# Kernel tuning notes

Measured on AMD Instinct MI355X. Metric: run time of the kernel, lower is better.

The kernel has to match this reference:

```python
import jax, jax.numpy as jnp
import numpy as np


def setup_inputs() -> dict:
    key = jax.random.key(0)
    k1, k2 = jax.random.split(key)
    B, L, D = 16, 512, 256
    text_features = jax.random.normal(k1, (B, L, D), dtype=jnp.float32)
    durations = jax.random.randint(k2, (B, L), 0, 32, dtype=jnp.int64)
    return {"text_features": text_features, "durations": durations, "target_length": 8192}


def reference(text_features, durations, target_length):
    """Length-regulator: expand [B,L,d] phoneme features to [B,T,d] frames.

    Frame t of batch b copies phoneme p where cumsum(dur)[b,p-1] <= t < cumsum(dur)[b,p];
    frames past the total duration are zero (matches torch zeros-init + trim/pad to
    target_length, since padding with the last frame only occurs when the buffer was
    already target_length long in the original code path with target_length set).
    """
    B, L, D = text_features.shape
    T = target_length  # static python int -> jit-friendly fixed output length
    cum = jnp.cumsum(durations, axis=1)                      # [B, L]
    t = jnp.arange(T, dtype=cum.dtype)                       # [T]
    # first phoneme index p with cum[b,p] > t  (side='right')
    idx = jax.vmap(lambda c: jnp.searchsorted(c, t, side='right'))(cum)  # [B, T]
    idx = jnp.minimum(idx, L - 1)
    valid = t[None, :] < cum[:, -1:]                         # [B, T] frames within total dur
    gathered = jnp.take_along_axis(text_features, idx[:, :, None], axis=1)  # [B, T, D]
    return jnp.where(valid[:, :, None], gathered, jnp.zeros((), dtype=text_features.dtype))
```

## Files before the change

kernel.cpp:

```cpp
#include <hip/hip_runtime.h>

#define MAX_L 2048
#define MAX_EPC 8
#define FRAMES_PER_BLOCK 64

__global__ __launch_bounds__(256, 3) void lr_fused_kernel(
        const float* __restrict__ feat,
        const int* __restrict__ dur,
        const int* __restrict__ tlen,
        float* __restrict__ out,
        int BL, int BT, int D) {
    const int T = *tlen;
    const int B = BT / T;
    const int L = BL / B;
    const int vecs = D >> 2;

    __shared__ int sc[MAX_L];
    __shared__ int swsum[4];
    __shared__ int sidx[FRAMES_PER_BLOCK];

    const int frame_base = blockIdx.x * FRAMES_PER_BLOCK;
    if (frame_base >= BT) return;
    const int b  = frame_base / T;
    const int t0 = frame_base - b * T;

    const int tid  = threadIdx.x;
    const int lane = tid & 63;
    const int wv   = tid >> 6;

    const int epc  = (L + blockDim.x - 1) / blockDim.x;
    const int base = tid * epc;
    const int* __restrict__ drow = dur + (size_t)b * L;

    int local[MAX_EPC];
    int run = 0;
#pragma unroll
    for (int e = 0; e < MAX_EPC; ++e) {
        int v = 0;
        if (e < epc && base + e < L) v = drow[base + e];
        run += v;
        local[e] = run;
    }
    int ws = run;
#pragma unroll
    for (int off = 1; off < 64; off <<= 1) {
        int up = __shfl_up(ws, off, 64);
        if (lane >= off) ws += up;
    }
    if (lane == 63) swsum[wv] = ws;
    __syncthreads();
    int wprefix = 0;
    for (int w = 0; w < wv; ++w) wprefix += swsum[w];
    const int chunk_prefix = wprefix + ws - run;
#pragma unroll
    for (int e = 0; e < MAX_EPC; ++e) {
        if (e < epc && base + e < L) sc[base + e] = chunk_prefix + local[e];
    }
    __syncthreads();

    const int total = sc[L - 1];

    if (tid < FRAMES_PER_BLOCK) {
        const int t = t0 + tid;
        int p = -1;
        if (t < total && frame_base + tid < BT) {
            int lo = 0, hi = L - 1;
            while (lo < hi) {
                const int mid = (lo + hi) >> 1;
                if (sc[mid] > t) hi = mid;
                else             lo = mid + 1;
            }
            p = lo;
        }
        sidx[tid] = p;
    }
    __syncthreads();

    const float4 z = make_float4(0.f, 0.f, 0.f, 0.f);

    if (vecs == 64) {
        const float4* __restrict__ fb = (const float4*)(feat + (size_t)b * L * D);
        float4* __restrict__ ob = (float4*)(out + (size_t)frame_base * D);
#pragma unroll
        for (int j = 0; j < 16; ++j) {
            const int f  = wv * 16 + j;
            const int pj = sidx[f];
            float4 v = z;
            if (pj >= 0) v = fb[(size_t)pj * 64 + lane];
            ob[(size_t)f * 64 + lane] = v;
        }
    } else {
        const float4* __restrict__ fb = (const float4*)(feat + (size_t)b * L * D);
        float4* __restrict__ ob = (float4*)(out + (size_t)frame_base * D);
        for (int j = 0; j < 16; ++j) {
            const int f = wv * 16 + j;
            if (frame_base + f >= BT) continue;
            const int pj = sidx[f];
            float4* __restrict__ orow = ob + (size_t)f * vecs;
            if (pj >= 0) {
                const float4* __restrict__ irow = fb + (size_t)pj * vecs;
                for (int i = lane; i < vecs; i += 64) orow[i] = irow[i];
            } else {
                for (int i = lane; i < vecs; i += 64) orow[i] = z;
            }
        }
    }
}

extern "C" void kernel_launch(void* const* d_in, const int* in_sizes, int n_in,
                              void* d_out, int out_size, void* d_ws, size_t ws_size,
                              hipStream_t stream) {
    const float* feat = (const float*)d_in[0];
    const int*   dur  = (const int*)d_in[1];
    const int*   tlen = (const int*)d_in[2];

    const int BL = in_sizes[1];
    const int D  = in_sizes[0] / in_sizes[1];
    const int BT = out_size / D;

    const int grid = (BT + FRAMES_PER_BLOCK - 1) / FRAMES_PER_BLOCK;
    lr_fused_kernel<<<grid, 256, 0, stream>>>(feat, dur, tlen, (float*)d_out,
                                              BL, BT, D);
}
```

Measured before the change: 147.8 us.

## Split into index kernel and grid-stride float4 gather copy kernel

Splits the fused kernel in two. The first kernel computes the per-frame source row index: one frame per thread, with 256 frames per block so the prefix scan is shared across more frames. The second kernel does a flat grid-stride gather copy with 4-way unrolled float4 loads over a fixed grid of 2048 blocks. This cuts redundant per-block cumsum work and raises memory-level parallelism in the copy, at the cost of an extra launch and writing and reading the index array through global memory.

```diff
diff --git a/kernel.cpp b/kernel.cpp
--- a/kernel.cpp
+++ b/kernel.cpp
@@ -2,24 +2,20 @@
 
 #define MAX_L 2048
 #define MAX_EPC 8
-#define FRAMES_PER_BLOCK 64
 
-__global__ __launch_bounds__(256, 3) void lr_fused_kernel(
-        const float* __restrict__ feat,
+__global__ __launch_bounds__(256) void lr_index_kernel(
         const int* __restrict__ dur,
         const int* __restrict__ tlen,
-        float* __restrict__ out,
-        int BL, int BT, int D) {
+        int* __restrict__ widx,
+        int BL, int BT) {
     const int T = *tlen;
     const int B = BT / T;
     const int L = BL / B;
-    const int vecs = D >> 2;
 
     __shared__ int sc[MAX_L];
     __shared__ int swsum[4];
-    __shared__ int sidx[FRAMES_PER_BLOCK];
 
-    const int frame_base = blockIdx.x * FRAMES_PER_BLOCK;
+    const int frame_base = blockIdx.x * 256;
     if (frame_base >= BT) return;
     const int b  = frame_base / T;
     const int t0 = frame_base - b * T;
@@ -53,57 +49,74 @@
     for (int w = 0; w < wv; ++w) wprefix += swsum[w];
     const int chunk_prefix = wprefix + ws - run;
 #pragma unroll
-    for (int e = 0; e < MAX_EPC; ++e) {
+    for (int e = 0; e < MAX_EPC; ++e)
         if (e < epc && base + e < L) sc[base + e] = chunk_prefix + local[e];
-    }
     __syncthreads();
 
     const int total = sc[L - 1];
 
-    if (tid < FRAMES_PER_BLOCK) {
+    const int f = frame_base + tid;
+    if (f < BT) {
         const int t = t0 + tid;
         int p = -1;
-        if (t < total && frame_base + tid < BT) {
+        if (t < total) {
             int lo = 0, hi = L - 1;
             while (lo < hi) {
                 const int mid = (lo + hi) >> 1;
                 if (sc[mid] > t) hi = mid;
                 else             lo = mid + 1;
             }
-            p = lo;
+            p = b * L + lo;
         }
-        sidx[tid] = p;
+        widx[f] = p;
     }
-    __syncthreads();
+}
 
+__global__ __launch_bounds__(256) void lr_copy_kernel(
+        const float4* __restrict__ fb,
+        const int* __restrict__ widx,
+        float4* __restrict__ ob,
+        long n, int shift) {
+    const long stride = (long)gridDim.x * blockDim.x;
+    const int  mask   = (1 << shift) - 1;
     const float4 z = make_float4(0.f, 0.f, 0.f, 0.f);
 
-    if (vecs == 64) {
-        const float4* __restrict__ fb = (const float4*)(feat + (size_t)b * L * D);
-        float4* __restrict__ ob = (float4*)(out + (size_t)frame_base * D);
-#pragma unroll
-        for (int j = 0; j < 16; ++j) {
-            const int f  = wv * 16 + j;
-            const int pj = sidx[f];
-            float4 v = z;
-            if (pj >= 0) v = fb[(size_t)pj * 64 + lane];
-            ob[(size_t)f * 64 + lane] = v;
-        }
-    } else {
-        const float4* __restrict__ fb = (const float4*)(feat + (size_t)b * L * D);
-        float4* __restrict__ ob = (float4*)(out + (size_t)frame_base * D);
-        for (int j = 0; j < 16; ++j) {
-            const int f = wv * 16 + j;
-            if (frame_base + f >= BT) continue;
-            const int pj = sidx[f];
-            float4* __restrict__ orow = ob + (size_t)f * vecs;
-            if (pj >= 0) {
-                const float4* __restrict__ irow = fb + (size_t)pj * vecs;
-                for (int i = lane; i < vecs; i += 64) orow[i] = irow[i];
-            } else {
-                for (int i = lane; i < vecs; i += 64) orow[i] = z;
-            }
-        }
+    long g = (long)blockIdx.x * blockDim.x + threadIdx.x;
+    for (; g + 3 * stride < n; g += 4 * stride) {
+        const long g0 = g, g1 = g + stride, g2 = g + 2 * stride, g3 = g + 3 * stride;
+        const int r0 = widx[g0 >> shift];
+        const int r1 = widx[g1 >> shift];
+        const int r2 = widx[g2 >> shift];
+        const int r3 = widx[g3 >> shift];
+        float4 v0 = fb[((long)max(r0, 0) << shift) + (int)(g0 & mask)];
+        float4 v1 = fb[((long)max(r1, 0) << shift) + (int)(g1 & mask)];
+        float4 v2 = fb[((long)max(r2, 0) << shift) + (int)(g2 & mask)];
+        float4 v3 = fb[((long)max(r3, 0) << shift) + (int)(g3 & mask)];
+        ob[g0] = (r0 >= 0) ? v0 : z;
+        ob[g1] = (r1 >= 0) ? v1 : z;
+        ob[g2] = (r2 >= 0) ? v2 : z;
+        ob[g3] = (r3 >= 0) ? v3 : z;
+    }
+    for (; g < n; g += stride) {
+        const int r = widx[g >> shift];
+        float4 v = fb[((long)max(r, 0) << shift) + (int)(g & mask)];
+        ob[g] = (r >= 0) ? v : z;
+    }
+}
+
+__global__ __launch_bounds__(256) void lr_copy_generic_kernel(
+        const float4* __restrict__ fb,
+        const int* __restrict__ widx,
+        float4* __restrict__ ob,
+        long n, int vecs) {
+    const long stride = (long)gridDim.x * blockDim.x;
+    const float4 z = make_float4(0.f, 0.f, 0.f, 0.f);
+    for (long g = (long)blockIdx.x * blockDim.x + threadIdx.x; g < n; g += stride) {
+        const long frame = g / vecs;
+        const int  off   = (int)(g - frame * vecs);
+        const int  r     = widx[frame];
+        float4 v = fb[(long)max(r, 0) * vecs + off];
+        ob[g] = (r >= 0) ? v : z;
     }
 }
 
@@ -117,8 +130,25 @@
     const int BL = in_sizes[1];
     const int D  = in_sizes[0] / in_sizes[1];
     const int BT = out_size / D;
+    const int vecs = D >> 2;
 
-    const int grid = (BT + FRAMES_PER_BLOCK - 1) / FRAMES_PER_BLOCK;
-    lr_fused_kernel<<<grid, 256, 0, stream>>>(feat, dur, tlen, (float*)d_out,
-                                              BL, BT, D);
+    int* widx = (int*)d_ws;
+
+    const int grid1 = (BT + 255) / 256;
+    lr_index_kernel<<<grid1, 256, 0, stream>>>(dur, tlen, widx, BL, BT);
+
+    const long n = (long)BT * vecs;
+    int shift = -1;
+    if ((vecs & (vecs - 1)) == 0) {
+        shift = 0;
+        while ((1 << shift) != vecs) ++shift;
+    }
+    const int grid2 = 2048;
+    if (shift >= 0) {
+        lr_copy_kernel<<<grid2, 256, 0, stream>>>(
+            (const float4*)feat, widx, (float4*)d_out, n, shift);
+    } else {
+        lr_copy_generic_kernel<<<grid2, 256, 0, stream>>>(
+            (const float4*)feat, widx, (float4*)d_out, n, vecs);
+    }
 }
```

Result: slower. 185.3 us (+25.3%).

## Double frames per block and reuse loaded rows across repeated phoneme indices

Applied to the files above, without the earlier changes.

Each block now handles 128 frames instead of 64, which halves the number of blocks that each recompute the per-batch duration prefix scan. The fast path broadcasts each frame's phoneme index with readlane and reloads the feature row only when the index changes, cutting redundant global reads for consecutive frames that map to the same phoneme. Blocks can now span a batch boundary through a segment loop. The occupancy hint in launch_bounds was removed, and with fewer blocks the GPU has less parallelism to hide memory latency.

```diff
diff --git a/kernel.cpp b/kernel.cpp
--- a/kernel.cpp
+++ b/kernel.cpp
@@ -2,9 +2,9 @@
 
 #define MAX_L 2048
 #define MAX_EPC 8
-#define FRAMES_PER_BLOCK 64
+#define FPB 128
 
-__global__ __launch_bounds__(256, 3) void lr_fused_kernel(
+__global__ __launch_bounds__(256) void lr_fused_kernel(
         const float* __restrict__ feat,
         const int* __restrict__ dur,
         const int* __restrict__ tlen,
@@ -17,93 +17,107 @@
 
     __shared__ int sc[MAX_L];
     __shared__ int swsum[4];
-    __shared__ int sidx[FRAMES_PER_BLOCK];
+    __shared__ int sidx[FPB];
 
-    const int frame_base = blockIdx.x * FRAMES_PER_BLOCK;
-    if (frame_base >= BT) return;
-    const int b  = frame_base / T;
-    const int t0 = frame_base - b * T;
+    const long frame_base0 = (long)blockIdx.x * FPB;
+    if (frame_base0 >= BT) return;
 
     const int tid  = threadIdx.x;
     const int lane = tid & 63;
     const int wv   = tid >> 6;
 
-    const int epc  = (L + blockDim.x - 1) / blockDim.x;
-    const int base = tid * epc;
-    const int* __restrict__ drow = dur + (size_t)b * L;
+    long fb_ = frame_base0;
+    int remaining = (int)((long)BT - frame_base0 < FPB ? (long)BT - frame_base0
+                                                       : (long)FPB);
 
-    int local[MAX_EPC];
-    int run = 0;
+    while (remaining > 0) {
+        const int b   = (int)(fb_ / T);
+        const int tt0 = (int)(fb_ - (long)b * T);
+        const int seg = remaining < (T - tt0) ? remaining : (T - tt0);
+
+        __syncthreads();
+        const int epc  = (L + blockDim.x - 1) / blockDim.x;
+        const int base = tid * epc;
+        const int* __restrict__ drow = dur + (size_t)b * L;
+        int local[MAX_EPC];
+        int run = 0;
 #pragma unroll
-    for (int e = 0; e < MAX_EPC; ++e) {
-        int v = 0;
-        if (e < epc && base + e < L) v = drow[base + e];
-        run += v;
-        local[e] = run;
-    }
-    int ws = run;
+        for (int e = 0; e < MAX_EPC; ++e) {
+            int v = 0;
+            if (e < epc && base + e < L) v = drow[base + e];
+            run += v;
+            local[e] = run;
+        }
+        int wsum = run;
 #pragma unroll
-    for (int off = 1; off < 64; off <<= 1) {
-        int up = __shfl_up(ws, off, 64);
-        if (lane >= off) ws += up;
-    }
-    if (lane == 63) swsum[wv] = ws;
-    __syncthreads();
-    int wprefix = 0;
-    for (int w = 0; w < wv; ++w) wprefix += swsum[w];
-    const int chunk_prefix = wprefix + ws - run;
+        for (int off = 1; off < 64; off <<= 1) {
+            int up = __shfl_up(wsum, off, 64);
+            if (lane >= off) wsum += up;
+        }
+        if (lane == 63) swsum[wv] = wsum;
+        __syncthreads();
+        int wprefix = 0;
+        for (int w = 0; w < wv; ++w) wprefix += swsum[w];
+        const int chunk_prefix = wprefix + wsum - run;
 #pragma unroll
-    for (int e = 0; e < MAX_EPC; ++e) {
-        if (e < epc && base + e < L) sc[base + e] = chunk_prefix + local[e];
-    }
-    __syncthreads();
+        for (int e = 0; e < MAX_EPC; ++e)
+            if (e < epc && base + e < L) sc[base + e] = chunk_prefix + local[e];
+        __syncthreads();
 
-    const int total = sc[L - 1];
+        const int total = sc[L - 1];
 
-    if (tid < FRAMES_PER_BLOCK) {
-        const int t = t0 + tid;
-        int p = -1;
-        if (t < total && frame_base + tid < BT) {
-            int lo = 0, hi = L - 1;
-            while (lo < hi) {
-                const int mid = (lo + hi) >> 1;
-                if (sc[mid] > t) hi = mid;
-                else             lo = mid + 1;
+        if (tid < seg) {
+            const int t = tt0 + tid;
+            int p = -1;
+            if (t < total) {
+                int lo = 0, hi = L - 1;
+                while (lo < hi) {
+                    const int mid = (lo + hi) >> 1;
+                    if (sc[mid] > t) hi = mid;
+                    else             lo = mid + 1;
+                }
+                p = lo;
             }
-            p = lo;
+            sidx[tid] = p;
         }
-        sidx[tid] = p;
-    }
-    __syncthreads();
+        __syncthreads();
 
-    const float4 z = make_float4(0.f, 0.f, 0.f, 0.f);
-
-    if (vecs == 64) {
-        const float4* __restrict__ fb = (const float4*)(feat + (size_t)b * L * D);
-        float4* __restrict__ ob = (float4*)(out + (size_t)frame_base * D);
+        if (seg == FPB && vecs == 64) {
+            const float4* __restrict__ fbp =
+                (const float4*)feat + (size_t)b * L * 64;
+            float4* __restrict__ op =
+                (float4*)out + ((size_t)fb_ + (size_t)wv * 32) * 64 + lane;
+            const int si = sidx[wv * 32 + (lane & 31)];
+            int prev = -2;
+            float4 v = make_float4(0.f, 0.f, 0.f, 0.f);
 #pragma unroll
-        for (int j = 0; j < 16; ++j) {
-            const int f  = wv * 16 + j;
-            const int pj = sidx[f];
-            float4 v = z;
-            if (pj >= 0) v = fb[(size_t)pj * 64 + lane];
-            ob[(size_t)f * 64 + lane] = v;
-        }
-    } else {
-        const float4* __restrict__ fb = (const float4*)(feat + (size_t)b * L * D);
-        float4* __restrict__ ob = (float4*)(out + (size_t)frame_base * D);
-        for (int j = 0; j < 16; ++j) {
-            const int f = wv * 16 + j;
-            if (frame_base + f >= BT) continue;
-            const int pj = sidx[f];
-            float4* __restrict__ orow = ob + (size_t)f * vecs;
-            if (pj >= 0) {
-                const float4* __restrict__ irow = fb + (size_t)pj * vecs;
-                for (int i = lane; i < vecs; i += 64) orow[i] = irow[i];
-            } else {
-                for (int i = lane; i < vecs; i += 64) orow[i] = z;
+            for (int j = 0; j < 32; ++j) {
+                const int p = __builtin_amdgcn_readlane(si, j);
+                if (p != prev) {
+                    v = (p >= 0) ? fbp[(size_t)p * 64 + lane]
+                                 : make_float4(0.f, 0.f, 0.f, 0.f);
+                    prev = p;
+                }
+                op[(size_t)j * 64] = v;
+            }
+        } else {
+            const float4* __restrict__ fbp =
+                (const float4*)feat + (size_t)b * L * vecs;
+            const float4 z = make_float4(0.f, 0.f, 0.f, 0.f);
+            for (int f = wv; f < seg; f += 4) {
+                const int p = sidx[f];
+                float4* __restrict__ orow = (float4*)out + ((size_t)fb_ + f) * vecs;
+                if (p >= 0) {
+                    const float4* __restrict__ irow = fbp + (size_t)p * vecs;
+                    for (int i = lane; i < vecs; i += 64) orow[i] = irow[i];
+                } else {
+                    for (int i = lane; i < vecs; i += 64) orow[i] = z;
+                }
             }
         }
+
+        fb_ += seg;
+        remaining -= seg;
     }
 }
 
@@ -118,7 +132,7 @@
     const int D  = in_sizes[0] / in_sizes[1];
     const int BT = out_size / D;
 
-    const int grid = (BT + FRAMES_PER_BLOCK - 1) / FRAMES_PER_BLOCK;
+    const int grid = (BT + FPB - 1) / FPB;
     lr_fused_kernel<<<grid, 256, 0, stream>>>(feat, dur, tlen, (float*)d_out,
                                               BL, BT, D);
 }
```

After: 144.9 us. No clear change (-1.9%).
